# Kernel tuning notes

Measured on AMD Instinct MI355X. Metric: run time of the kernel, lower is better.

## Reference

```python
import jax, jax.numpy as jnp
import numpy as np

M0, M1 = 16, 8          # scalar / vector multiplicities (16x0e + 8x1o)
NB = 16                  # number_of_basis
RMAX = 8.0               # max_radius
N_NODES, N_EDGES = 10000, 160000
WNUM = M0*M0 + M0*M1 + M1*M1 + M1*M0  # 576, tp weight_numel


def sus(t):
    """e3nn soft_unit_step: exp(-1/t) for t>0 else 0."""
    safe = jnp.where(t > 0, t, 1.0)
    return jnp.where(t > 0, jnp.exp(-1.0 / safe), 0.0)


def setup_inputs():
    key = jax.random.key(0)
    ks = jax.random.split(key, 12)
    D = M0 + 3 * M1  # 40
    x = jax.random.normal(ks[0], (N_NODES, D), jnp.float32)
    edge_index = jax.random.randint(ks[1], (2, N_EDGES), 0, N_NODES, jnp.int32)
    edge_attr = jax.random.normal(ks[2], (N_EDGES, 4), jnp.float32)  # sh lmax=1
    node_attr = jnp.ones((N_NODES, 1), jnp.float32)
    batch = jnp.zeros((N_NODES,), jnp.int32)
    amf = jax.random.uniform(ks[3], (N_EDGES, 1), jnp.float32) * RMAX  # edge lengths
    Wq0 = jax.random.normal(ks[4], (M0, M0), jnp.float32)
    Wq1 = jax.random.normal(ks[5], (M1, M1), jnp.float32)
    Wk1 = jax.random.normal(ks[6], (NB, 16), jnp.float32)
    Wk2 = jax.random.normal(ks[7], (16, WNUM), jnp.float32)
    Wv1 = jax.random.normal(ks[8], (NB, 16), jnp.float32)
    Wv2 = jax.random.normal(ks[9], (16, WNUM), jnp.float32)
    Wd0 = jax.random.normal(ks[10], (M0, M0), jnp.float32)
    Wd1 = jax.random.normal(ks[11], (M1, M1), jnp.float32)
    return dict(x=x, edge_index=edge_index, edge_attr=edge_attr, node_attr=node_attr,
                batch=batch, additional_message_features=amf,
                Wq0=Wq0, Wq1=Wq1, Wk1=Wk1, Wk2=Wk2, Wv1=Wv1, Wv2=Wv2, Wd0=Wd0, Wd1=Wd1)


def reference(x, edge_index, edge_attr, node_attr, batch, additional_message_features,
              Wq0, Wq1, Wk1, Wk2, Wv1, Wv2, Wd0, Wd1):
    n = x.shape[0]
    src, dst = edge_index[0], edge_index[1]
    d = additional_message_features.reshape(-1)  # [E]

    # soft_one_hot_linspace(basis='smooth_finite', cutoff=True) * sqrt(NB)
    centers = jnp.linspace(0.0, RMAX, NB + 2)[1:-1]
    step = RMAX / (NB + 1)
    diff = (d[:, None] - centers) / step
    emb = (1.14136 * np.exp(2.0)) * sus(diff + 1.0) * sus(1.0 - diff) * np.sqrt(NB)  # [E,NB]
    cutoff = sus(10.0 * (1.0 - d / RMAX))  # [E]

    # split irreps: scalars [*,M0], vectors [*,M1,3]
    x0 = x[:, :M0]
    x1 = x[:, M0:].reshape(n, M1, 3)

    # q = Linear(input_irreps -> hidden_irreps): per-irrep linear, 1/sqrt(fan_in)
    q0 = (x0 @ Wq0) / np.sqrt(M0)
    q1 = jnp.einsum('nui,uw->nwi', x1, Wq1) / np.sqrt(M1)

    # radial MLPs producing per-edge tensor-product weights
    def radial(W1, W2):
        h = jax.nn.silu((emb @ W1) / np.sqrt(NB))
        return (h @ W2) / np.sqrt(16.0)  # [E, WNUM]
    wk = radial(Wk1, Wk2)
    wv = radial(Wv1, Wv2)

    xs0, xs1 = x0[src], x1[src]           # gather by edge source
    sh0, sh1 = edge_attr[:, 0], edge_attr[:, 1:4]
    dot11 = jnp.einsum('eui,ei->eu', xs1, sh1) / np.sqrt(3.0)  # 1o x 1o -> 0e CG

    def fctp(w):
        # FullyConnectedTensorProduct(input, sh, out) with per-edge weights.
        s1 = M0 * M0
        s2 = s1 + M0 * M1
        s3 = s2 + M1 * M1
        w1 = w[:, :s1].reshape(-1, M0, M0)   # 0e x 0e -> 0e
        w2 = w[:, s1:s2].reshape(-1, M0, M1) # 0e x 1o -> 1o
        w3 = w[:, s2:s3].reshape(-1, M1, M1) # 1o x 0e -> 1o
        w4 = w[:, s3:].reshape(-1, M1, M0)   # 1o x 1o -> 0e
        norm = 1.0 / np.sqrt(M0 + M1)        # path fan-in normalization
        o0 = (jnp.einsum('euw,eu->ew', w1, xs0 * sh0[:, None]) +
              jnp.einsum('euw,eu->ew', w4, dot11)) * norm            # [E,M0]
        o1 = (jnp.einsum('euw,eu,ei->ewi', w2, xs0, sh1) +
              jnp.einsum('euw,eui->ewi', w3, xs1 * sh0[:, None, None])) * norm  # [E,M1,3]
        return o0, o1

    k0, k1 = fctp(wk)
    v0, v1 = fctp(wv)

    # dot: FullyConnectedTensorProduct(hidden, hidden, '0e') with shared weights
    score = (jnp.einsum('eu,ev,uv->e', q0[dst], k0, Wd0) +
             jnp.einsum('eui,evi,uv->e', q1[dst], k1, Wd1) / np.sqrt(3.0)) / np.sqrt(M0*M0 + M1*M1)

    expv = cutoff * jnp.exp(score)                                   # [E]
    z = jax.ops.segment_sum(expv, dst, num_segments=n)               # [N]
    z = jnp.where(z == 0, 1.0, z)
    alpha = expv / z[dst]
    we = jnp.sqrt(jax.nn.relu(alpha))                                # alpha.relu().sqrt()
    v = jnp.concatenate([v0, v1.reshape(-1, 3 * M1)], axis=1)        # [E,40]
    return jax.ops.segment_sum(we[:, None] * v, dst, num_segments=n) # [N,40]
```

## Files before the change

kernel.cpp:

```cpp
#include <hip/hip_runtime.h>
#include <hip/hip_bf16.h>

#define E_CNT 160000
#define N_CNT 10000

#define INV_STEP   2.125f
#define EMB_C      33.734292f
#define INVS320    0.05590170f
#define INVS8      0.35355339f
#define INV_SQRT3  0.57735027f
#define KSCALE     0.051031036f

#define OFF_FLAG   0
#define OFF_XF     16
#define OFF_EAF    400016
#define OFF_AMFF   1040016
#define OFF_WQ0F   1200016
#define OFF_WQ1F   1200272
#define OFF_WD0F   1200336
#define OFF_WD1F   1200592
#define OFF_WK1F   1200656
#define OFF_WV1F   1200912
#define OFF_WK2F   1201168
#define OFF_WV2F   1210384
#define OFF_P      1219600
#define OFF_EXPV   1619600
#define OFF_VBUF   1779600
#define OFF_DEG    8179600
#define OFF_Z      8179600
#define OFF_DEG2   8189600
#define OFF_START  8199600
#define OFF_START2 8209601
#define OFF_CURS   8219602
#define OFF_CURS2  8229602
#define OFF_ELIST  8239602
#define OFF_ELIST2 8399602
#define OFF_G      8559632

static __device__ __forceinline__ float bf2f(__hip_bfloat16 b) { return __bfloat162float(b); }
static __device__ __forceinline__ float sanitize(float v) {
    return fminf(fmaxf(v, -1e30f), 1e30f);
}
static __device__ __forceinline__ unsigned short f2bf(float f) {
    unsigned x = __float_as_uint(f);
    unsigned r = (x + 0x7fffu + ((x >> 16) & 1u)) >> 16;
    return (unsigned short)r;
}
static __device__ __forceinline__ float bflo(unsigned u) { return __uint_as_float(u << 16); }
static __device__ __forceinline__ float bfhi(unsigned u) { return __uint_as_float(u & 0xffff0000u); }

__global__ __launch_bounds__(256) void prep_kernel(
    const void* __restrict__ x,   const void* __restrict__ ea,  const void* __restrict__ amf,
    const void* __restrict__ Wq0, const void* __restrict__ Wq1,
    const void* __restrict__ Wk1, const void* __restrict__ Wk2,
    const void* __restrict__ Wv1, const void* __restrict__ Wv2,
    const void* __restrict__ Wd0, const void* __restrict__ Wd1,
    const int* __restrict__ ei, float* __restrict__ ws)
{
    __shared__ int sflag;
    const int tid = threadIdx.x;
    if (tid == 0) {
        const unsigned short* xb = (const unsigned short*)x;
        int cnt = 0;
        for (int k = 0; k < 256; k += 2) {
            unsigned e = (unsigned)((xb[k] >> 7) & 0xFF);
            if (e >= 141) ++cnt;
        }
        sflag = (cnt >= 8) ? 1 : 0;
        if (blockIdx.x == 0) *(int*)ws = sflag;
    }
    __syncthreads();
    const int f32 = sflag;
    const int i = blockIdx.x * 256 + tid;
#define CV(p, idx) (f32 ? ((const float*)(p))[idx] : bf2f(((const __hip_bfloat16*)(p))[idx]))
    if (i < 400000) ws[OFF_XF + i]   = CV(x, i);
    if (i < 640000) ws[OFF_EAF + i]  = CV(ea, i);
    if (i < 160000) {
        ws[OFF_AMFF + i] = CV(amf, i);
        atomicAdd((int*)(ws + OFF_DEG)  + ei[E_CNT + i], 1);
        atomicAdd((int*)(ws + OFF_DEG2) + ei[i], 1);
    }
    if (i < 9216) { ws[OFF_WK2F + i] = CV(Wk2, i); ws[OFF_WV2F + i] = CV(Wv2, i); }
    if (i < 256) {
        ws[OFF_WQ0F + i] = CV(Wq0, i); ws[OFF_WD0F + i] = CV(Wd0, i);
        ws[OFF_WK1F + i] = CV(Wk1, i); ws[OFF_WV1F + i] = CV(Wv1, i);
    }
    if (i < 64) { ws[OFF_WQ1F + i] = CV(Wq1, i); ws[OFF_WD1F + i] = CV(Wd1, i); }
#undef CV
}

__global__ __launch_bounds__(512) void scan_kernel(float* __restrict__ ws)
{
    __shared__ int ssum[512];
    const int t    = threadIdx.x;
    const int half = t >> 8;
    const int lt   = t & 255;
    int* deg   = (int*)(ws + (half ? OFF_DEG2   : OFF_DEG));
    int* start = (int*)(ws + (half ? OFF_START2 : OFF_START));
    int* curs  = (int*)(ws + (half ? OFF_CURS2  : OFF_CURS));
    const int base = lt * 40;
    int s = 0;
    for (int k = 0; k < 40; ++k) {
        int idx = base + k;
        if (idx < N_CNT) s += deg[idx];
    }
    ssum[t] = s;
    __syncthreads();
    for (int off = 1; off < 256; off <<= 1) {
        int v = (lt >= off) ? ssum[t - off] : 0;
        __syncthreads();
        ssum[t] += v;
        __syncthreads();
    }
    int run = ssum[t] - s;
    for (int k = 0; k < 40; ++k) {
        int idx = base + k;
        if (idx < N_CNT) {
            start[idx] = run;
            curs[idx]  = run;
            run += deg[idx];
        }
    }
    if (lt == 255) start[N_CNT] = E_CNT;
    __syncthreads();
    for (int k = t; k < N_CNT; k += 512) ws[OFF_Z + k] = 0.f;
}

__global__ __launch_bounds__(256) void fillgp_kernel(const int* __restrict__ ei, float* __restrict__ ws)
{
    const int blk = blockIdx.x;
    const int tid = threadIdx.x;
    if (blk < 625) {
        const int e = blk * 256 + tid;
        int pd = atomicAdd((int*)(ws + OFF_CURS)  + ei[E_CNT + e], 1);
        ((int*)(ws + OFF_ELIST))[pd] = e;
        int ps = atomicAdd((int*)(ws + OFF_CURS2) + ei[e], 1);
        ((int*)(ws + OFF_ELIST2))[ps] = e;
        return;
    }
    if (blk >= 1875) {
        const int n = (blk - 1875) * 256 + tid;
        if (n >= N_CNT) return;
        const float* WQ0 = ws + OFF_WQ0F;
        const float* WQ1 = ws + OFF_WQ1F;
        const float* WD0 = ws + OFF_WD0F;
        const float* WD1 = ws + OFF_WD1F;
        float xs[40];
        const float4* xr = (const float4*)(ws + OFF_XF + n * 40);
#pragma unroll
        for (int k = 0; k < 10; ++k) {
            float4 f = xr[k];
            xs[4 * k + 0] = f.x; xs[4 * k + 1] = f.y; xs[4 * k + 2] = f.z; xs[4 * k + 3] = f.w;
        }
        float q0[16];
#pragma unroll
        for (int w = 0; w < 16; ++w) {
            float s = 0.f;
#pragma unroll
            for (int u = 0; u < 16; ++u) s = fmaf(xs[u], WQ0[u * 16 + w], s);
            q0[w] = s * 0.25f;
        }
        float* pn = ws + OFF_P + n * 40;
#pragma unroll
        for (int v = 0; v < 16; ++v) {
            float s = 0.f;
#pragma unroll
            for (int w = 0; w < 16; ++w) s = fmaf(q0[w], WD0[w * 16 + v], s);
            pn[v] = sanitize(s * INVS320);
        }
        float q1[24];
#pragma unroll
        for (int w = 0; w < 8; ++w) {
            float s0 = 0.f, s1 = 0.f, s2 = 0.f;
#pragma unroll
            for (int u = 0; u < 8; ++u) {
                float wq = WQ1[u * 8 + w];
                s0 = fmaf(xs[16 + u * 3 + 0], wq, s0);
                s1 = fmaf(xs[16 + u * 3 + 1], wq, s1);
                s2 = fmaf(xs[16 + u * 3 + 2], wq, s2);
            }
            q1[w * 3 + 0] = s0 * INVS8;
            q1[w * 3 + 1] = s1 * INVS8;
            q1[w * 3 + 2] = s2 * INVS8;
        }
#pragma unroll
        for (int v = 0; v < 8; ++v) {
            float s0 = 0.f, s1 = 0.f, s2 = 0.f;
#pragma unroll
            for (int w = 0; w < 8; ++w) {
                float wd = WD1[w * 8 + v];
                s0 = fmaf(q1[w * 3 + 0], wd, s0);
                s1 = fmaf(q1[w * 3 + 1], wd, s1);
                s2 = fmaf(q1[w * 3 + 2], wd, s2);
            }
            const float sc = INVS320 * INV_SQRT3;
            pn[16 + v * 3 + 0] = sanitize(s0 * sc);
            pn[16 + v * 3 + 1] = sanitize(s1 * sc);
            pn[16 + v * 3 + 2] = sanitize(s2 * sc);
        }
        return;
    }
    const int t = (blk - 625) * 256 + tid;
    const int p   = t / 160000;
    const int rem = t - p * 160000;
    const int c   = rem / 10000;
    const int n   = rem - c * 10000;

    const float* W2 = ws + (p ? OFF_WV2F : OFF_WK2F) + c * 576;
    const float* xv = ws + OFF_XF + n * 40;
    float x0[16], x1[24];
#pragma unroll
    for (int u = 0; u < 16; ++u) x0[u] = xv[u];
#pragma unroll
    for (int u = 0; u < 24; ++u) x1[u] = xv[16 + u];

    float out[96];
#pragma unroll
    for (int w = 0; w < 16; ++w) {
        float s = 0.f;
#pragma unroll
        for (int u = 0; u < 16; ++u) s = fmaf(W2[u * 16 + w], x0[u], s);
        out[w] = s;
    }
#pragma unroll
    for (int w = 0; w < 8; ++w) {
        float s = 0.f;
#pragma unroll
        for (int u = 0; u < 16; ++u) s = fmaf(W2[256 + u * 8 + w], x0[u], s);
        out[16 + w] = s;
    }
#pragma unroll
    for (int w = 0; w < 8; ++w) {
        float s0 = 0.f, s1 = 0.f, s2 = 0.f;
#pragma unroll
        for (int u = 0; u < 8; ++u) {
            float wv = W2[384 + u * 8 + w];
            s0 = fmaf(wv, x1[u * 3 + 0], s0);
            s1 = fmaf(wv, x1[u * 3 + 1], s1);
            s2 = fmaf(wv, x1[u * 3 + 2], s2);
        }
        out[24 + w * 3 + 0] = s0;
        out[24 + w * 3 + 1] = s1;
        out[24 + w * 3 + 2] = s2;
    }
#pragma unroll
    for (int w = 0; w < 16; ++w) {
        float s0 = 0.f, s1 = 0.f, s2 = 0.f;
#pragma unroll
        for (int u = 0; u < 8; ++u) {
            float wv = W2[448 + u * 16 + w];
            s0 = fmaf(wv, x1[u * 3 + 0], s0);
            s1 = fmaf(wv, x1[u * 3 + 1], s1);
            s2 = fmaf(wv, x1[u * 3 + 2], s2);
        }
        out[48 + w * 3 + 0] = s0 * INV_SQRT3;
        out[48 + w * 3 + 1] = s1 * INV_SQRT3;
        out[48 + w * 3 + 2] = s2 * INV_SQRT3;
    }

    uint4 ov[12];
    unsigned* ou = (unsigned*)ov;
#pragma unroll
    for (int k = 0; k < 48; ++k)
        ou[k] = (unsigned)f2bf(out[2 * k]) | ((unsigned)f2bf(out[2 * k + 1]) << 16);
    uint4* dp = (uint4*)((unsigned short*)(ws + OFF_G) + ((size_t)n * 2 + p) * 1536 + c * 96);
#pragma unroll
    for (int q = 0; q < 12; ++q) dp[q] = ov[q];
}

static __device__ __forceinline__ void load48(unsigned (&ub)[48], const uint4* __restrict__ rp)
{
#pragma unroll
    for (int q = 0; q < 12; ++q) {
        uint4 v = rp[q];
        ub[4 * q + 0] = v.x; ub[4 * q + 1] = v.y;
        ub[4 * q + 2] = v.z; ub[4 * q + 3] = v.w;
    }
}

static __device__ __forceinline__ void accum48(const unsigned (&ub)[48], float hc, float sh0,
    float s1x, float s1y, float s1z,
    float (&o0)[16], float (&o1)[24], float (&t2a)[8])
{
    const float hs = hc * sh0;
#define GVAL(k) (((k) & 1) ? bfhi(ub[(k) >> 1]) : bflo(ub[(k) >> 1]))
#pragma unroll
    for (int w = 0; w < 16; ++w) o0[w] = fmaf(hs, GVAL(w), o0[w]);
#pragma unroll
    for (int w = 0; w < 8; ++w) t2a[w] = fmaf(hc, GVAL(16 + w), t2a[w]);
#pragma unroll
    for (int w = 0; w < 8; ++w) {
        o1[w * 3 + 0] = fmaf(hs, GVAL(24 + w * 3 + 0), o1[w * 3 + 0]);
        o1[w * 3 + 1] = fmaf(hs, GVAL(24 + w * 3 + 1), o1[w * 3 + 1]);
        o1[w * 3 + 2] = fmaf(hs, GVAL(24 + w * 3 + 2), o1[w * 3 + 2]);
    }
#pragma unroll
    for (int w = 0; w < 16; ++w) {
        float g = GVAL(48 + w * 3 + 0) * s1x;
        g = fmaf(GVAL(48 + w * 3 + 1), s1y, g);
        g = fmaf(GVAL(48 + w * 3 + 2), s1z, g);
        o0[w] = fmaf(hc, g, o0[w]);
    }
#undef GVAL
}

__global__ __launch_bounds__(256, 2) void edge_kernel(
    const int* __restrict__ ei, float* __restrict__ ws)
{
    __shared__ float h_s[16 * 256];
    const int tid  = threadIdx.x;
    const int pass = tid >> 7;
    const int lane = tid & 127;
    const int b  = blockIdx.x;
    const int lb = (b < 1248) ? ((b & 7) * 156 + (b >> 3)) : b;
    const int sidx = lb * 128 + lane;
    const int e    = ((const int*)(ws + OFF_ELIST2))[sidx];
    const int src  = ei[e];
    const int dst  = ei[E_CNT + e];

    const float d   = ws[OFF_AMFF + e];
    const float dsv = d * INV_STEP;
    float emb[16];
#pragma unroll
    for (int bb = 0; bb < 16; ++bb) {
        float t1 = dsv - (float)bb;
        float t2 = (float)(bb + 2) - dsv;
        float v = 0.f;
        if (t1 > 0.f && t2 > 0.f) v = EMB_C * expf(-1.f / t1 - 1.f / t2);
        emb[bb] = v;
    }

    const float* W1 = ws + (pass ? OFF_WV1F : OFF_WK1F);
#pragma unroll 1
    for (int j = 0; j < 16; ++j) {
        float s = 0.f;
#pragma unroll
        for (int bb = 0; bb < 16; ++bb) s = fmaf(emb[bb], W1[bb * 16 + j], s);
        s *= 0.25f;
        h_s[j * 256 + tid] = s / (1.f + expf(-s));
    }

    const float4 eav = ((const float4*)(ws + OFF_EAF))[e];
    const float sh0 = eav.x, s1x = eav.y, s1y = eav.z, s1z = eav.w;

    float o0[16], o1[24], t2a[8];
#pragma unroll
    for (int i = 0; i < 16; ++i) o0[i] = 0.f;
#pragma unroll
    for (int i = 0; i < 24; ++i) o1[i] = 0.f;
#pragma unroll
    for (int i = 0; i < 8; ++i) t2a[i] = 0.f;

    const uint4* Gp = (const uint4*)((const unsigned short*)(ws + OFF_G)
                                     + ((size_t)src * 2 + pass) * 1536);

    unsigned A[48], B[48];
    load48(A, Gp);
#pragma unroll 1
    for (int c = 0; c < 16; c += 2) {
        load48(B, Gp + (c + 1) * 12);
        accum48(A, h_s[c * 256 + tid], sh0, s1x, s1y, s1z, o0, o1, t2a);
        if (c + 2 < 16) load48(A, Gp + (c + 2) * 12);
        accum48(B, h_s[(c + 1) * 256 + tid], sh0, s1x, s1y, s1z, o0, o1, t2a);
    }

#pragma unroll
    for (int w = 0; w < 8; ++w) {
        o1[w * 3 + 0] = fmaf(t2a[w], s1x, o1[w * 3 + 0]);
        o1[w * 3 + 1] = fmaf(t2a[w], s1y, o1[w * 3 + 1]);
        o1[w * 3 + 2] = fmaf(t2a[w], s1z, o1[w * 3 + 2]);
    }

    if (pass == 0) {
        const float* pd = ws + OFF_P + dst * 40;
        float sc = 0.f;
#pragma unroll
        for (int j = 0; j < 16; ++j) sc = fmaf(o0[j], pd[j], sc);
#pragma unroll
        for (int j = 0; j < 24; ++j) sc = fmaf(o1[j], pd[16 + j], sc);
        sc = fminf(fmaxf(sc * KSCALE, -60.f), 60.f);
        float ct = 10.f * (1.f - d * 0.125f);
        float cutoff = (ct > 0.f) ? expf(-1.f / ct) : 0.f;
        float ev = fmaxf(cutoff * expf(sc), 0.f);
        ws[OFF_EXPV + e] = ev;
        atomicAdd(ws + OFF_Z + dst, ev);
    } else {
        float* vr = ws + OFF_VBUF + (size_t)e * 40;
#pragma unroll
        for (int j = 0; j < 16; ++j) vr[j] = sanitize(o0[j] * KSCALE);
#pragma unroll
        for (int j = 0; j < 24; ++j) vr[16 + j] = sanitize(o1[j] * KSCALE);
    }
}

__global__ __launch_bounds__(256) void gather_kernel(
    const float* __restrict__ ws, void* __restrict__ out)
{
    const int i = blockIdx.x * 256 + threadIdx.x;
    if (i >= N_CNT * 40) return;
    const int n = i / 40;
    const int f = i - n * 40;
    const int* start = (const int*)(ws + OFF_START);
    const int* elist = (const int*)(ws + OFF_ELIST);
    const float* expv = ws + OFF_EXPV;
    const float* Vbuf = ws + OFF_VBUF;
    const int s = start[n], t = start[n + 1];

    float zz = ws[OFF_Z + n];
    const float rz = (zz > 0.f) ? 1.f / zz : 1.f;

    float acc = 0.f;
    for (int j = s; j < t; ++j) {
        const int e = elist[j];
        const float we = sqrtf(fmaxf(expv[e] * rz, 0.f));
        acc = fmaf(we, Vbuf[(size_t)e * 40 + f], acc);
    }
    acc = sanitize(acc);
    const int f32 = *(const int*)ws;
    if (f32) ((float*)out)[i] = acc;
    else     ((__hip_bfloat16*)out)[i] = __float2bfloat16(acc);
}

extern "C" void kernel_launch(void* const* d_in, const int* in_sizes, int n_in,
                              void* d_out, int out_size, void* d_ws, size_t ws_size,
                              hipStream_t stream)
{
    (void)in_sizes; (void)n_in; (void)out_size; (void)ws_size;
    const void* x   = d_in[0];
    const int*  ei  = (const int*)d_in[1];
    const void* ea  = d_in[2];
    const void* amf = d_in[5];
    const void* Wq0 = d_in[6];
    const void* Wq1 = d_in[7];
    const void* Wk1 = d_in[8];
    const void* Wk2 = d_in[9];
    const void* Wv1 = d_in[10];
    const void* Wv2 = d_in[11];
    const void* Wd0 = d_in[12];
    const void* Wd1 = d_in[13];

    float* ws = (float*)d_ws;

    hipMemsetAsync(ws + OFF_DEG, 0, 20000 * sizeof(int), stream);
    prep_kernel<<<2500, 256, 0, stream>>>(x, ea, amf, Wq0, Wq1, Wk1, Wk2, Wv1, Wv2, Wd0, Wd1, ei, ws);
    scan_kernel<<<1, 512, 0, stream>>>(ws);
    fillgp_kernel<<<1915, 256, 0, stream>>>(ei, ws);
    edge_kernel<<<1250, 256, 0, stream>>>(ei, ws);
    gather_kernel<<<(N_CNT * 40 + 255) / 256, 256, 0, stream>>>(ws, d_out);
}
```

Measured before the change: 322.5 us.

## Write edge outputs in dst-sorted order and vectorize input conversion

The edge kernel now writes expv and the value rows at each edge's position in the destination-sorted list, found through a new dpos array built during the fill pass. This lets the gather kernel read expv and Vbuf contiguously without an elist indirection. The prep kernel converts inputs four elements per thread with vector loads and launches fewer blocks, and the fillgp node loads use float4. The cost is an extra int read per edge, and edge-kernel writes become scattered.

```diff
diff --git a/kernel.cpp b/kernel.cpp
--- a/kernel.cpp
+++ b/kernel.cpp
@@ -33,7 +33,7 @@
 #define OFF_START2 8209601
 #define OFF_CURS   8219602
 #define OFF_CURS2  8229602
-#define OFF_ELIST  8239602
+#define OFF_DPOS   8239602
 #define OFF_ELIST2 8399602
 #define OFF_G      8559632
 
@@ -48,6 +48,16 @@
 }
 static __device__ __forceinline__ float bflo(unsigned u) { return __uint_as_float(u << 16); }
 static __device__ __forceinline__ float bfhi(unsigned u) { return __uint_as_float(u & 0xffff0000u); }
+
+static __device__ __forceinline__ float4 load4(const void* p, int i4, int f32)
+{
+    if (f32) return ((const float4*)p)[i4];
+    uint2 u = ((const uint2*)p)[i4];
+    float4 r;
+    r.x = bflo(u.x); r.y = bfhi(u.x);
+    r.z = bflo(u.y); r.w = bfhi(u.y);
+    return r;
+}
 
 __global__ __launch_bounds__(256) void prep_kernel(
     const void* __restrict__ x,   const void* __restrict__ ea,  const void* __restrict__ amf,
@@ -72,21 +82,31 @@
     __syncthreads();
     const int f32 = sflag;
     const int i = blockIdx.x * 256 + tid;
-#define CV(p, idx) (f32 ? ((const float*)(p))[idx] : bf2f(((const __hip_bfloat16*)(p))[idx]))
-    if (i < 400000) ws[OFF_XF + i]   = CV(x, i);
-    if (i < 640000) ws[OFF_EAF + i]  = CV(ea, i);
-    if (i < 160000) {
-        ws[OFF_AMFF + i] = CV(amf, i);
-        atomicAdd((int*)(ws + OFF_DEG)  + ei[E_CNT + i], 1);
-        atomicAdd((int*)(ws + OFF_DEG2) + ei[i], 1);
-    }
-    if (i < 9216) { ws[OFF_WK2F + i] = CV(Wk2, i); ws[OFF_WV2F + i] = CV(Wv2, i); }
-    if (i < 256) {
-        ws[OFF_WQ0F + i] = CV(Wq0, i); ws[OFF_WD0F + i] = CV(Wd0, i);
-        ws[OFF_WK1F + i] = CV(Wk1, i); ws[OFF_WV1F + i] = CV(Wv1, i);
-    }
-    if (i < 64) { ws[OFF_WQ1F + i] = CV(Wq1, i); ws[OFF_WD1F + i] = CV(Wd1, i); }
-#undef CV
+
+    if (i < 100000) ((float4*)(ws + OFF_XF))[i] = load4(x, i, f32);
+    if (i < 160000) ((float4*)(ws + OFF_EAF))[i] = load4(ea, i, f32);
+    if (i < 40000)  ((float4*)(ws + OFF_AMFF))[i] = load4(amf, i, f32);
+    if (i < 40000) {
+#pragma unroll
+        for (int k = 0; k < 4; ++k) {
+            atomicAdd((int*)(ws + OFF_DEG)  + ei[E_CNT + 4 * i + k], 1);
+            atomicAdd((int*)(ws + OFF_DEG2) + ei[4 * i + k], 1);
+        }
+    }
+    if (i < 2304) {
+        ((float4*)(ws + OFF_WK2F))[i] = load4(Wk2, i, f32);
+        ((float4*)(ws + OFF_WV2F))[i] = load4(Wv2, i, f32);
+    }
+    if (i < 64) {
+        ((float4*)(ws + OFF_WQ0F))[i] = load4(Wq0, i, f32);
+        ((float4*)(ws + OFF_WD0F))[i] = load4(Wd0, i, f32);
+        ((float4*)(ws + OFF_WK1F))[i] = load4(Wk1, i, f32);
+        ((float4*)(ws + OFF_WV1F))[i] = load4(Wv1, i, f32);
+    }
+    if (i < 16) {
+        ((float4*)(ws + OFF_WQ1F))[i] = load4(Wq1, i, f32);
+        ((float4*)(ws + OFF_WD1F))[i] = load4(Wd1, i, f32);
+    }
 }
 
 __global__ __launch_bounds__(512) void scan_kernel(float* __restrict__ ws)
@@ -133,9 +153,9 @@
     if (blk < 625) {
         const int e = blk * 256 + tid;
         int pd = atomicAdd((int*)(ws + OFF_CURS)  + ei[E_CNT + e], 1);
-        ((int*)(ws + OFF_ELIST))[pd] = e;
         int ps = atomicAdd((int*)(ws + OFF_CURS2) + ei[e], 1);
         ((int*)(ws + OFF_ELIST2))[ps] = e;
+        ((int*)(ws + OFF_DPOS))[ps]   = pd;
         return;
     }
     if (blk >= 1875) {
@@ -207,12 +227,20 @@
     const int n   = rem - c * 10000;
 
     const float* W2 = ws + (p ? OFF_WV2F : OFF_WK2F) + c * 576;
-    const float* xv = ws + OFF_XF + n * 40;
     float x0[16], x1[24];
-#pragma unroll
-    for (int u = 0; u < 16; ++u) x0[u] = xv[u];
-#pragma unroll
-    for (int u = 0; u < 24; ++u) x1[u] = xv[16 + u];
+    {
+        const float4* xr = (const float4*)(ws + OFF_XF + n * 40);
+        float xs[40];
+#pragma unroll
+        for (int k = 0; k < 10; ++k) {
+            float4 f = xr[k];
+            xs[4 * k + 0] = f.x; xs[4 * k + 1] = f.y; xs[4 * k + 2] = f.z; xs[4 * k + 3] = f.w;
+        }
+#pragma unroll
+        for (int u = 0; u < 16; ++u) x0[u] = xs[u];
+#pragma unroll
+        for (int u = 0; u < 24; ++u) x1[u] = xs[16 + u];
+    }
 
     float out[96];
 #pragma unroll
@@ -315,6 +343,7 @@
     const int lb = (b < 1248) ? ((b & 7) * 156 + (b >> 3)) : b;
     const int sidx = lb * 128 + lane;
     const int e    = ((const int*)(ws + OFF_ELIST2))[sidx];
+    const int dpos = ((const int*)(ws + OFF_DPOS))[sidx];
     const int src  = ei[e];
     const int dst  = ei[E_CNT + e];
 
@@ -382,10 +411,10 @@
         float ct = 10.f * (1.f - d * 0.125f);
         float cutoff = (ct > 0.f) ? expf(-1.f / ct) : 0.f;
         float ev = fmaxf(cutoff * expf(sc), 0.f);
-        ws[OFF_EXPV + e] = ev;
+        ws[OFF_EXPV + dpos] = ev;
         atomicAdd(ws + OFF_Z + dst, ev);
     } else {
-        float* vr = ws + OFF_VBUF + (size_t)e * 40;
+        float* vr = ws + OFF_VBUF + (size_t)dpos * 40;
 #pragma unroll
         for (int j = 0; j < 16; ++j) vr[j] = sanitize(o0[j] * KSCALE);
 #pragma unroll
@@ -401,7 +430,6 @@
     const int n = i / 40;
     const int f = i - n * 40;
     const int* start = (const int*)(ws + OFF_START);
-    const int* elist = (const int*)(ws + OFF_ELIST);
     const float* expv = ws + OFF_EXPV;
     const float* Vbuf = ws + OFF_VBUF;
     const int s = start[n], t = start[n + 1];
@@ -411,9 +439,8 @@
 
     float acc = 0.f;
     for (int j = s; j < t; ++j) {
-        const int e = elist[j];
-        const float we = sqrtf(fmaxf(expv[e] * rz, 0.f));
-        acc = fmaf(we, Vbuf[(size_t)e * 40 + f], acc);
+        const float we = sqrtf(fmaxf(expv[j] * rz, 0.f));
+        acc = fmaf(we, Vbuf[(size_t)j * 40 + f], acc);
     }
     acc = sanitize(acc);
     const int f32 = *(const int*)ws;
@@ -442,7 +469,7 @@
     float* ws = (float*)d_ws;
 
     hipMemsetAsync(ws + OFF_DEG, 0, 20000 * sizeof(int), stream);
-    prep_kernel<<<2500, 256, 0, stream>>>(x, ea, amf, Wq0, Wq1, Wk1, Wk2, Wv1, Wv2, Wd0, Wd1, ei, ws);
+    prep_kernel<<<625, 256, 0, stream>>>(x, ea, amf, Wq0, Wq1, Wk1, Wk2, Wv1, Wv2, Wd0, Wd1, ei, ws);
     scan_kernel<<<1, 512, 0, stream>>>(ws);
     fillgp_kernel<<<1915, 256, 0, stream>>>(ei, ws);
     edge_kernel<<<1250, 256, 0, stream>>>(ei, ws);
```

Result: faster. 310.1 us (-3.9%).
